# Kernel tuning notes

Hardware: AMD Instinct MI355X
Metric: run time of the kernel (lower is better)

The kernel has to match this reference:

```python
import jax, jax.numpy as jnp
import numpy as np

N_NODES = 50000
N_EDGES = 800000
IN_DIM, HID_DIM, OUT_DIM = 128, 128, 64


def setup_inputs() -> dict:
    key = jax.random.key(0)
    ks = jax.random.split(key, 8)
    x = jax.random.normal(ks[0], (N_NODES, IN_DIM), dtype=jnp.float32)
    edge_index = jax.random.randint(ks[1], (2, N_EDGES), 0, N_NODES, dtype=jnp.int64)
    # GCNConv uses Glorot weights + zero bias; any random init is fine for a reference
    W1 = jax.random.normal(ks[2], (IN_DIM, HID_DIM), dtype=jnp.float32) / np.sqrt(IN_DIM)
    b1 = jnp.zeros((HID_DIM,), dtype=jnp.float32)
    W2 = jax.random.normal(ks[3], (HID_DIM, OUT_DIM), dtype=jnp.float32) / np.sqrt(HID_DIM)
    b2 = jnp.zeros((OUT_DIM,), dtype=jnp.float32)
    Wfc = jax.random.normal(ks[4], (OUT_DIM, 2), dtype=jnp.float32) / np.sqrt(OUT_DIM)
    bfc = jnp.zeros((2,), dtype=jnp.float32)
    return {"x": x, "edge_index": edge_index, "W1": W1, "b1": b1,
            "W2": W2, "b2": b2, "Wfc": Wfc, "bfc": bfc}


def _gcn_conv(x, src, dst, W, b, n_nodes):
    """PyG GCNConv: out = D^{-1/2} (A+I) D^{-1/2} (x W) + b."""
    xw = x @ W  # [N, F_out] transform before propagation
    ones = jnp.ones(src.shape[0], dtype=xw.dtype)
    deg = jax.ops.segment_sum(ones, dst, num_segments=n_nodes) + 1.0  # +1 for self-loop
    dinv = jax.lax.rsqrt(deg)
    norm = dinv[src] * dinv[dst]  # [E]
    msg = xw[src] * norm[:, None]  # gather + scale: [E, F_out]
    agg = jax.ops.segment_sum(msg, dst, num_segments=n_nodes)  # scatter-add
    agg = agg + xw * (dinv * dinv)[:, None]  # self-loop contribution (norm = 1/deg)
    return agg + b


def reference(x, edge_index, W1, b1, W2, b2, Wfc, bfc):
    n = x.shape[0]
    src, dst = edge_index[0], edge_index[1]
    h = jax.nn.relu(_gcn_conv(x, src, dst, W1, b1, n))
    # dropout is identity in eval mode
    h = _gcn_conv(h, src, dst, W2, b2, n)
    h = h @ Wfc + bfc
    return jax.nn.leaky_relu(h, negative_slope=0.01)
```

## Files before the change

### kernel.cpp

```cpp
#include <hip/hip_runtime.h>
#include <hip/hip_fp16.h>

#define IN_DIM 128
#define HID_DIM 128
#define OUT_DIM 64
#define BINW 128
#define BINSHIFT 7
#define MAXBIN 512
#define CAP 4096
#define CNTSTRIDE 16
#define SC_GRID 256

typedef _Float16 f16x8 __attribute__((ext_vector_type(8)));
typedef float f32x4 __attribute__((ext_vector_type(4)));

__global__ __launch_bounds__(256) void k_build_gemm(const float* __restrict__ x,
                                                    const float* __restrict__ W,
                                                    __half* __restrict__ xwh,
                                                    const int* __restrict__ src,
                                                    const int* __restrict__ dst,
                                                    int* __restrict__ bin_cnt,
                                                    int* __restrict__ ovf_cnt,
                                                    unsigned int* __restrict__ ovf,
                                                    unsigned int* __restrict__ ebin,
                                                    int N, int E, int nbin) {
    __shared__ union SMem {
        unsigned int wt_raw[8192];
        struct { int h[MAXBIN]; int base_s[MAXBIN]; } sc;
    } smem;
    const int nGemm = (N + 127) >> 7;
    int tid = threadIdx.x;

    if ((int)blockIdx.x < nGemm) {
        char* wb = (char*)smem.wt_raw;
        {
            int kk0 = (tid & 15) * 2;
            int c8  = (tid >> 4) * 8;
#pragma unroll
            for (int i = 0; i < 4; ++i) {
                int kk = i * 32 + kk0;
                const float* w0 = W + (size_t)kk * HID_DIM + c8;
                const float* w1 = w0 + HID_DIM;
                float4 a0 = *(const float4*)w0;
                float4 a1 = *(const float4*)(w0 + 4);
                float4 b0 = *(const float4*)w1;
                float4 b1 = *(const float4*)(w1 + 4);
                float va[8] = {a0.x, a0.y, a0.z, a0.w, a1.x, a1.y, a1.z, a1.w};
                float vb[8] = {b0.x, b0.y, b0.z, b0.w, b1.x, b1.y, b1.z, b1.w};
#pragma unroll
                for (int j = 0; j < 8; ++j) {
                    int col = c8 + j;
                    int byte = (col << 8) + (kk << 1);
                    byte ^= ((col & 7) << 4);
                    *(__half2*)(wb + byte) = __floats2half2_rn(va[j], vb[j]);
                }
            }
        }
        int lane = tid & 63;
        int wv   = tid >> 6;
        int lcol = lane & 15;
        int lk   = (lane >> 4) << 3;
        int swz  = (lcol & 7) << 4;
        int rb   = blockIdx.x * 128 + wv * 32;
        int rows[2];
        const float* xp[2];
#pragma unroll
        for (int r = 0; r < 2; ++r) {
            int row = rb + 16 * r + lcol;
            rows[r] = row;
            if (row > N - 1) row = N - 1;
            xp[r] = x + (size_t)row * IN_DIM + lk;
        }
        f32x4 acc[2][8];
#pragma unroll
        for (int r = 0; r < 2; ++r)
#pragma unroll
            for (int c = 0; c < 8; ++c) acc[r][c] = (f32x4){0.f, 0.f, 0.f, 0.f};

        __syncthreads();

        auto mk = [](float4 f0, float4 f1, f16x8& hi, f16x8& lo) {
            float f[8] = {f0.x, f0.y, f0.z, f0.w, f1.x, f1.y, f1.z, f1.w};
#pragma unroll
            for (int e = 0; e < 8; ++e) {
                _Float16 h = (_Float16)f[e];
                hi[e] = h;
                lo[e] = (_Float16)(f[e] - (float)h);
            }
        };
#pragma unroll
        for (int kc = 0; kc < 4; ++kc) {
            f16x8 xhi[2], xlo[2];
#pragma unroll
            for (int r = 0; r < 2; ++r) {
                float4 f0 = *(const float4*)(xp[r] + kc * 32);
                float4 f1 = *(const float4*)(xp[r] + kc * 32 + 4);
                mk(f0, f1, xhi[r], xlo[r]);
            }
#pragma unroll
            for (int c = 0; c < 8; ++c) {
                int ad = ((c << 12) | (lcol << 8) | ((kc << 6) + (lk << 1))) ^ swz;
                f16x8 wfrag = *(const f16x8*)(wb + ad);
                acc[0][c] = __builtin_amdgcn_mfma_f32_16x16x32_f16(wfrag, xhi[0], acc[0][c], 0, 0, 0);
                acc[0][c] = __builtin_amdgcn_mfma_f32_16x16x32_f16(wfrag, xlo[0], acc[0][c], 0, 0, 0);
                acc[1][c] = __builtin_amdgcn_mfma_f32_16x16x32_f16(wfrag, xhi[1], acc[1][c], 0, 0, 0);
                acc[1][c] = __builtin_amdgcn_mfma_f32_16x16x32_f16(wfrag, xlo[1], acc[1][c], 0, 0, 0);
            }
        }
        int cq = lane >> 4;
#pragma unroll
        for (int r = 0; r < 2; ++r) {
            if (rows[r] < N) {
                uint2* p = (uint2*)(xwh + (size_t)rows[r] * HID_DIM);
#pragma unroll
                for (int c = 0; c < 8; ++c) {
                    union { __half2 h[2]; uint2 u; } pk;
                    pk.h[0] = __floats2half2_rn(acc[r][c].x, acc[r][c].y);
                    pk.h[1] = __floats2half2_rn(acc[r][c].z, acc[r][c].w);
                    p[4 * c + cq] = pk.u;
                }
            }
        }
    } else {
        int sb = blockIdx.x - nGemm;
        int* h = smem.sc.h;
        int* base_s = smem.sc.base_s;
        for (int k = tid; k < nbin; k += 256) h[k] = 0;
        __syncthreads();
        int per = E / SC_GRID;
        int ebeg = sb * per;
        int eend = (sb + 1 == SC_GRID) ? E : ebeg + per;
        for (int i = ebeg + tid; i < eend; i += 256)
            atomicAdd(&h[dst[i] >> BINSHIFT], 1);
        __syncthreads();
        for (int k = tid; k < nbin; k += 256) {
            int c = h[k];
            base_s[k] = (c > 0) ? atomicAdd(&bin_cnt[k * CNTSTRIDE], c) : 0;
            h[k] = 0;
        }
        __syncthreads();
        for (int i = ebeg + tid; i < eend; i += 256) {
            unsigned int s = (unsigned int)src[i];
            unsigned int d = (unsigned int)dst[i];
            int b = (int)(d >> BINSHIFT);
            int pos = base_s[b] + atomicAdd(&h[b], 1);
            unsigned int packed = s | (d << 16);
            if (pos < CAP) ebin[(size_t)b * CAP + pos] = packed;
            else ovf[atomicAdd(ovf_cnt, 1)] = packed;
        }
    }
}

__global__ __launch_bounds__(256) void k_fill(const unsigned int* __restrict__ ebin,
                                              const int* __restrict__ bin_cnt,
                                              const int* __restrict__ ovf_cnt,
                                              const unsigned int* __restrict__ ovf,
                                              int* __restrict__ row_ptr,
                                              unsigned short* __restrict__ degu,
                                              unsigned short* __restrict__ csr_src,
                                              float* __restrict__ dinv,
                                              const float* __restrict__ W2,
                                              const float* __restrict__ Wfc,
                                              const float* __restrict__ b2,
                                              const float* __restrict__ bfc,
                                              float* __restrict__ Wc,
                                              float* __restrict__ bc,
                                              int N, int nbin) {
    __shared__ int cnt[BINW];
    __shared__ int excl[BINW];
    __shared__ int start[BINW];
    int k = blockIdx.x;
    int node0 = k * BINW;
    int nn = min(BINW, N - node0);
    int t = threadIdx.x;
    if (t < BINW) cnt[t] = 0;
    __syncthreads();
    int cnt_k = min(bin_cnt[k * CNTSTRIDE], CAP);
    const unsigned int* seg = ebin + (size_t)k * CAP;
    for (int i = t; i < cnt_k; i += 256)
        atomicAdd(&cnt[(seg[i] >> 16) & (BINW - 1)], 1);
    int novf = *ovf_cnt;
    for (int i = t; i < novf; i += 256) {
        unsigned int e = ovf[i];
        if ((int)(e >> (16 + BINSHIFT)) == k)
            atomicAdd(&cnt[(e >> 16) & (BINW - 1)], 1);
    }
    __syncthreads();
    if (t < BINW) excl[t] = (t < nn) ? cnt[t] : 0;
    __syncthreads();
    for (int off = 1; off < BINW; off <<= 1) {
        int u = 0;
        if (t < BINW && t >= off) u = excl[t - off];
        __syncthreads();
        if (t < BINW) excl[t] += u;
        __syncthreads();
    }
    if (t < nn) {
        int deg = cnt[t];
        int e0 = k * CAP + excl[t] - deg;
        start[t] = e0;
        row_ptr[node0 + t] = e0;
        degu[node0 + t] = (unsigned short)deg;
        dinv[node0 + t] = rsqrtf((float)deg + 1.0f);
        cnt[t] = 0;
    }
    __syncthreads();
    for (int i = t; i < cnt_k; i += 256) {
        unsigned int e = seg[i];
        int dl = (e >> 16) & (BINW - 1);
        int slot = start[dl] + atomicAdd(&cnt[dl], 1);
        csr_src[slot] = (unsigned short)(e & 0xffffu);
    }
    for (int i = t; i < novf; i += 256) {
        unsigned int e = ovf[i];
        if ((int)(e >> (16 + BINSHIFT)) == k) {
            int dl = (e >> 16) & (BINW - 1);
            int slot = start[dl] + atomicAdd(&cnt[dl], 1);
            csr_src[slot] = (unsigned short)(e & 0xffffu);
        }
    }
    if (k == 0) {
        int kk = t >> 1, j = t & 1;
        float acc = 0.f;
#pragma unroll 8
        for (int m = 0; m < OUT_DIM; ++m) acc += W2[kk * OUT_DIM + m] * Wfc[m * 2 + j];
        Wc[kk * 2 + j] = acc;
        if (kk == 0) {
            float b = 0.f;
#pragma unroll 8
            for (int m = 0; m < OUT_DIM; ++m) b += b2[m] * Wfc[m * 2 + j];
            bc[j] = b + bfc[j];
        }
    }
}

__global__ __launch_bounds__(256) void k_agg1z(const int* __restrict__ row_ptr,
                                               const unsigned short* __restrict__ degu,
                                               const unsigned short* __restrict__ csr_src,
                                               const float* __restrict__ dinv,
                                               const __half* __restrict__ xwh,
                                               const float* __restrict__ b1,
                                               const float* __restrict__ Wc,
                                               float* __restrict__ z, int N) {
    constexpr int F = HID_DIM;
    constexpr int L = F / 8;
    constexpr int EPW = 64 / L;
    __shared__ float Wcs[HID_DIM * 2];
    int tid = threadIdx.x;
    if (tid < 64) ((float4*)Wcs)[tid] = ((const float4*)Wc)[tid];
    __syncthreads();
    int node = (blockIdx.x * 256 + tid) >> 6;
    if (node >= N) return;
    int lane = tid & 63;
    int sub = lane / L;
    int c   = lane % L;
    int beg = row_ptr[node];
    int end = beg + degu[node];
    float dd = dinv[node];
    uint4 us = *(const uint4*)(xwh + (size_t)node * F + c * 8);
    float4 b1a = *(const float4*)(b1 + c * 8);
    float4 b1b = *(const float4*)(b1 + c * 8 + 4);
    float a0 = 0.f, a1 = 0.f, a2 = 0.f, a3 = 0.f;
    float a4 = 0.f, a5 = 0.f, a6 = 0.f, a7 = 0.f;
    auto acc = [&](uint4 u, float w) {
        float2 v0 = __half22float2(*(__half2*)&u.x);
        float2 v1 = __half22float2(*(__half2*)&u.y);
        float2 v2 = __half22float2(*(__half2*)&u.z);
        float2 v3 = __half22float2(*(__half2*)&u.w);
        a0 = fmaf(v0.x, w, a0); a1 = fmaf(v0.y, w, a1);
        a2 = fmaf(v1.x, w, a2); a3 = fmaf(v1.y, w, a3);
        a4 = fmaf(v2.x, w, a4); a5 = fmaf(v2.y, w, a5);
        a6 = fmaf(v3.x, w, a6); a7 = fmaf(v3.y, w, a7);
    };
    int j = beg + sub;
    for (; j + 3 * EPW < end; j += 4 * EPW) {
        int s0 = csr_src[j];
        int s1 = csr_src[j + EPW];
        int s2 = csr_src[j + 2 * EPW];
        int s3 = csr_src[j + 3 * EPW];
        uint4 u0 = *(const uint4*)(xwh + (size_t)s0 * F + c * 8);
        uint4 u1 = *(const uint4*)(xwh + (size_t)s1 * F + c * 8);
        uint4 u2 = *(const uint4*)(xwh + (size_t)s2 * F + c * 8);
        uint4 u3 = *(const uint4*)(xwh + (size_t)s3 * F + c * 8);
        float w0 = dinv[s0];
        float w1 = dinv[s1];
        float w2 = dinv[s2];
        float w3 = dinv[s3];
        acc(u0, w0); acc(u1, w1); acc(u2, w2); acc(u3, w3);
    }
    for (; j < end; j += EPW) {
        int s = csr_src[j];
        uint4 u = *(const uint4*)(xwh + (size_t)s * F + c * 8);
        acc(u, dinv[s]);
    }
#pragma unroll
    for (int off = L; off < 64; off <<= 1) {
        a0 += __shfl_xor(a0, off); a1 += __shfl_xor(a1, off);
        a2 += __shfl_xor(a2, off); a3 += __shfl_xor(a3, off);
        a4 += __shfl_xor(a4, off); a5 += __shfl_xor(a5, off);
        a6 += __shfl_xor(a6, off); a7 += __shfl_xor(a7, off);
    }
    float2 v0 = __half22float2(*(__half2*)&us.x);
    float2 v1 = __half22float2(*(__half2*)&us.y);
    float2 v2 = __half22float2(*(__half2*)&us.z);
    float2 v3 = __half22float2(*(__half2*)&us.w);
    float h[8];
    h[0] = fmaxf(fmaf(fmaf(v0.x, dd, a0), dd, b1a.x), 0.f);
    h[1] = fmaxf(fmaf(fmaf(v0.y, dd, a1), dd, b1a.y), 0.f);
    h[2] = fmaxf(fmaf(fmaf(v1.x, dd, a2), dd, b1a.z), 0.f);
    h[3] = fmaxf(fmaf(fmaf(v1.y, dd, a3), dd, b1a.w), 0.f);
    h[4] = fmaxf(fmaf(fmaf(v2.x, dd, a4), dd, b1b.x), 0.f);
    h[5] = fmaxf(fmaf(fmaf(v2.y, dd, a5), dd, b1b.y), 0.f);
    h[6] = fmaxf(fmaf(fmaf(v3.x, dd, a6), dd, b1b.z), 0.f);
    h[7] = fmaxf(fmaf(fmaf(v3.y, dd, a7), dd, b1b.w), 0.f);
    float o0 = 0.f, o1 = 0.f;
#pragma unroll
    for (int k = 0; k < 8; ++k) {
        o0 += h[k] * Wcs[(c * 8 + k) * 2 + 0];
        o1 += h[k] * Wcs[(c * 8 + k) * 2 + 1];
    }
#pragma unroll
    for (int off = 1; off < L; off <<= 1) {
        o0 += __shfl_xor(o0, off);
        o1 += __shfl_xor(o1, off);
    }
    if (lane == 0) {
        float2 r; r.x = o0 * dd; r.y = o1 * dd;
        *(float2*)(z + (size_t)node * 2) = r;
    }
}

__global__ __launch_bounds__(256) void k_agg2(const int* __restrict__ row_ptr,
                                              const unsigned short* __restrict__ degu,
                                              const unsigned short* __restrict__ csr_src,
                                              const float* __restrict__ dinv,
                                              const float* __restrict__ z,
                                              const float* __restrict__ bc,
                                              float* __restrict__ out, int N) {
    int tid = threadIdx.x;
    int gwave = (blockIdx.x * 256 + tid) >> 6;
    int lane = tid & 63;
    int grp = lane >> 3, li = lane & 7;
    int node = gwave * 8 + grp;
    if (node >= N) return;
    int beg = row_ptr[node];
    int end = beg + degu[node];
    float s0 = 0.f, s1 = 0.f;
    int j = beg + li;
    for (; j + 8 < end; j += 16) {
        int sa = csr_src[j];
        int sb = csr_src[j + 8];
        float2 za = *(const float2*)(z + (size_t)sa * 2);
        float2 zb = *(const float2*)(z + (size_t)sb * 2);
        s0 += za.x + zb.x; s1 += za.y + zb.y;
    }
    if (j < end) {
        int s = csr_src[j];
        float2 zv = *(const float2*)(z + (size_t)s * 2);
        s0 += zv.x; s1 += zv.y;
    }
#pragma unroll
    for (int off = 1; off < 8; off <<= 1) {
        s0 += __shfl_xor(s0, off);
        s1 += __shfl_xor(s1, off);
    }
    if (li == 0) {
        float2 zs = *(const float2*)(z + (size_t)node * 2);
        float dd = dinv[node];
        float o0 = (s0 + zs.x) * dd + bc[0];
        float o1 = (s1 + zs.y) * dd + bc[1];
        float2 r;
        r.x = o0 > 0.f ? o0 : 0.01f * o0;
        r.y = o1 > 0.f ? o1 : 0.01f * o1;
        *(float2*)(out + (size_t)node * 2) = r;
    }
}

extern "C" void kernel_launch(void* const* d_in, const int* in_sizes, int n_in,
                              void* d_out, int out_size, void* d_ws, size_t ws_size,
                              hipStream_t stream) {
    const float* x   = (const float*)d_in[0];
    const int*   ei  = (const int*)d_in[1];
    const float* W1  = (const float*)d_in[2];
    const float* b1  = (const float*)d_in[3];
    const float* W2  = (const float*)d_in[4];
    const float* b2  = (const float*)d_in[5];
    const float* Wfc = (const float*)d_in[6];
    const float* bfc = (const float*)d_in[7];

    const int N = in_sizes[0] / IN_DIM;
    const int E = in_sizes[1] / 2;
    const int* src = ei;
    const int* dst = ei + E;
    const int nbin = (N + BINW - 1) / BINW;

    char* base = (char*)d_ws;
    size_t off = 0;
    auto take = [&](size_t bytes) { size_t o = off; off = (off + bytes + 255) & ~(size_t)255; return (void*)(base + o); };
    int*    row_ptr  = (int*)take((size_t)N * 4);
    unsigned short* degu = (unsigned short*)take((size_t)N * 2);
    unsigned short* csr_src = (unsigned short*)take((size_t)nbin * CAP * 2);
    int*    bin_cnt  = (int*)take((size_t)(nbin * CNTSTRIDE + CNTSTRIDE) * 4);
    int*    ovf_cnt  = bin_cnt + nbin * CNTSTRIDE;
    unsigned int* ovf = (unsigned int*)take((size_t)E * 4);
    unsigned int* ebin = (unsigned int*)take((size_t)nbin * CAP * 4);
    float*  dinv     = (float*)take((size_t)N * 4);
    __half* xw1h     = (__half*)take((size_t)N * HID_DIM * 2);
    float*  zbuf     = (float*)take((size_t)N * 2 * 4);
    float*  Wc       = (float*)take((size_t)HID_DIM * 2 * 4);
    float*  bc       = (float*)take(2 * 4);

    hipMemsetAsync(bin_cnt, 0, (size_t)(nbin * CNTSTRIDE + CNTSTRIDE) * 4, stream);

    const int nGemm = (N + 127) / 128;
    k_build_gemm<<<nGemm + SC_GRID, 256, 0, stream>>>(x, W1, xw1h, src, dst, bin_cnt,
                                                      ovf_cnt, ovf, ebin, N, E, nbin);
    k_fill<<<nbin, 256, 0, stream>>>(ebin, bin_cnt, ovf_cnt, ovf, row_ptr, degu,
                                     csr_src, dinv, W2, Wfc, b2, bfc, Wc, bc, N, nbin);
    k_agg1z<<<(N + 3) / 4, 256, 0, stream>>>(row_ptr, degu, csr_src, dinv, xw1h, b1, Wc, zbuf, N);
    const int nAgg2 = ((N + 7) / 8 * 64 + 255) / 256;
    k_agg2<<<nAgg2, 256, 0, stream>>>(row_ptr, degu, csr_src, dinv, zbuf, bc, (float*)d_out, N);
}
```

Baseline: 156.0 us.

## Replace two-pass LDS binning with direct global atomics; stage bin segment in LDS

The edge-binning blocks drop the shared-memory histogram, the per-block reservation of bin offsets and the second pass. Each edge now reserves its slot directly with a global atomicAdd on the bin counter, using a grid-stride loop over a grid raised from 256 to 2048 blocks. This removes two block barriers and one full read of dst, but puts far more atomic traffic on a few hundred global counters. Separately, the fill kernel copies each bin's edge segment into shared memory once, so the two later passes read LDS instead of global memory.

```diff
diff --git a/kernel.cpp b/kernel.cpp
--- a/kernel.cpp
+++ b/kernel.cpp
@@ -9,7 +9,7 @@
 #define MAXBIN 512
 #define CAP 4096
 #define CNTSTRIDE 16
-#define SC_GRID 256
+#define SC_GRID 2048
 
 typedef _Float16 f16x8 __attribute__((ext_vector_type(8)));
 typedef float f32x4 __attribute__((ext_vector_type(4)));
@@ -24,15 +24,12 @@
                                                     unsigned int* __restrict__ ovf,
                                                     unsigned int* __restrict__ ebin,
                                                     int N, int E, int nbin) {
-    __shared__ union SMem {
-        unsigned int wt_raw[8192];
-        struct { int h[MAXBIN]; int base_s[MAXBIN]; } sc;
-    } smem;
+    __shared__ unsigned int wt_raw[8192];
     const int nGemm = (N + 127) >> 7;
     int tid = threadIdx.x;
 
     if ((int)blockIdx.x < nGemm) {
-        char* wb = (char*)smem.wt_raw;
+        char* wb = (char*)wt_raw;
         {
             int kk0 = (tid & 15) * 2;
             int c8  = (tid >> 4) * 8;
@@ -122,28 +119,13 @@
             }
         }
     } else {
-        int sb = blockIdx.x - nGemm;
-        int* h = smem.sc.h;
-        int* base_s = smem.sc.base_s;
-        for (int k = tid; k < nbin; k += 256) h[k] = 0;
-        __syncthreads();
-        int per = E / SC_GRID;
-        int ebeg = sb * per;
-        int eend = (sb + 1 == SC_GRID) ? E : ebeg + per;
-        for (int i = ebeg + tid; i < eend; i += 256)
-            atomicAdd(&h[dst[i] >> BINSHIFT], 1);
-        __syncthreads();
-        for (int k = tid; k < nbin; k += 256) {
-            int c = h[k];
-            base_s[k] = (c > 0) ? atomicAdd(&bin_cnt[k * CNTSTRIDE], c) : 0;
-            h[k] = 0;
-        }
-        __syncthreads();
-        for (int i = ebeg + tid; i < eend; i += 256) {
+        int i0 = (blockIdx.x - nGemm) * 256 + tid;
+        const int stride = SC_GRID * 256;
+        for (int i = i0; i < E; i += stride) {
             unsigned int s = (unsigned int)src[i];
             unsigned int d = (unsigned int)dst[i];
             int b = (int)(d >> BINSHIFT);
-            int pos = base_s[b] + atomicAdd(&h[b], 1);
+            int pos = atomicAdd(&bin_cnt[b * CNTSTRIDE], 1);
             unsigned int packed = s | (d << 16);
             if (pos < CAP) ebin[(size_t)b * CAP + pos] = packed;
             else ovf[atomicAdd(ovf_cnt, 1)] = packed;
@@ -169,16 +151,18 @@
     __shared__ int cnt[BINW];
     __shared__ int excl[BINW];
     __shared__ int start[BINW];
+    __shared__ unsigned int segl[CAP];
     int k = blockIdx.x;
     int node0 = k * BINW;
     int nn = min(BINW, N - node0);
     int t = threadIdx.x;
     if (t < BINW) cnt[t] = 0;
-    __syncthreads();
     int cnt_k = min(bin_cnt[k * CNTSTRIDE], CAP);
     const unsigned int* seg = ebin + (size_t)k * CAP;
+    for (int i = t; i < cnt_k; i += 256) segl[i] = seg[i];
+    __syncthreads();
     for (int i = t; i < cnt_k; i += 256)
-        atomicAdd(&cnt[(seg[i] >> 16) & (BINW - 1)], 1);
+        atomicAdd(&cnt[(segl[i] >> 16) & (BINW - 1)], 1);
     int novf = *ovf_cnt;
     for (int i = t; i < novf; i += 256) {
         unsigned int e = ovf[i];
@@ -206,7 +190,7 @@
     }
     __syncthreads();
     for (int i = t; i < cnt_k; i += 256) {
-        unsigned int e = seg[i];
+        unsigned int e = segl[i];
         int dl = (e >> 16) & (BINW - 1);
         int slot = start[dl] + atomicAdd(&cnt[dl], 1);
         csr_src[slot] = (unsigned short)(e & 0xffffu);
```

Result: slower. 177.2 us (+13.6%).
